# Kernel optimization log

Hardware: AMD Instinct MI355X
Metric: run time of the kernel (lower is better)

The kernel has to match this reference:

```python
import jax, jax.numpy as jnp
import numpy as np
from math import sqrt

MASK_SCALE = 128  # band half-width; entries with |i-j| < MASK_SCALE are masked to -inf

B, L, H, E = 4, 2048, 8, 64
D = 64


def setup_inputs() -> dict:
    key = jax.random.key(0)
    kq, kk, kv = jax.random.split(key, 3)
    queries = jax.random.normal(kq, (B, L, H, E), dtype=jnp.float32)
    keys = jax.random.normal(kk, (B, L, H, E), dtype=jnp.float32)
    values = jax.random.normal(kv, (B, L, H, D), dtype=jnp.float32)
    attn_mask = jnp.zeros((B, 1, L, L), dtype=bool)  # unused (mask_flag=False)
    return {"queries": queries, "keys": keys, "values": values, "attn_mask": attn_mask}


def reference(queries, keys, values, attn_mask):
    b, l, h, e = queries.shape
    scale = 1.0 / sqrt(e)
    # [B,H,L,S] dense scores
    scores = jnp.einsum('blhe,bshe->bhls', queries, keys)
    # create_diag_symmetric_mask(L, MASK_SCALE): 1 iff |i-j| < MASK_SCALE
    idx = jnp.arange(l)
    band = jnp.abs(idx[:, None] - idx[None, :]) < MASK_SCALE  # [L,L]
    # module masks the band to -inf (attends outside the band)
    scores = jnp.where(band[None, None, :, :], -jnp.inf, scores)
    A = jax.nn.softmax(scale * scores, axis=-1)
    V = jnp.einsum('bhls,bshd->blhd', A, values)
    return V
```

## Files before the change

kernel.cpp:

```cpp
#include <hip/hip_runtime.h>
#include <hip/hip_bf16.h>

typedef __bf16 bf16_t;
typedef __bf16 bf16x8 __attribute__((ext_vector_type(8)));
typedef float f32x4 __attribute__((ext_vector_type(4)));
typedef float f32x16 __attribute__((ext_vector_type(16)));
typedef unsigned int u32;

#define MFMA16(A,B,C) __builtin_amdgcn_mfma_f32_16x16x32_bf16(A,B,C,0,0,0)
#define MFMA32(A,B,C) __builtin_amdgcn_mfma_f32_32x32x16_bf16(A,B,C,0,0,0)

constexpr int Bb = 4, Ll = 2048, Hh = 8, Ee = 64, Dd = 64;
constexpr int LDP = 72;
constexpr int MS = 128;

static __device__ __forceinline__ bf16x8 cvt8(float4 a, float4 b) {
    bf16x8 t;
    t[0] = (bf16_t)a.x; t[1] = (bf16_t)a.y; t[2] = (bf16_t)a.z; t[3] = (bf16_t)a.w;
    t[4] = (bf16_t)b.x; t[5] = (bf16_t)b.y; t[6] = (bf16_t)b.z; t[7] = (bf16_t)b.w;
    return t;
}

static __device__ __forceinline__ u32 pkbf(float lo, float hi) {
    u32 d;
    asm("v_cvt_pk_bf16_f32 %0, %1, %2" : "=v"(d) : "v"(lo), "v"(hi));
    return d;
}

static __device__ __forceinline__ float fexp2(float x) {
    float r;
    asm("v_exp_f32 %0, %1" : "=v"(r) : "v"(x));
    return r;
}

static __device__ __forceinline__ f32x16 zero16() {
    f32x16 z;
    #pragma unroll
    for (int r = 0; r < 16; ++r) z[r] = 0.f;
    return z;
}

__global__ __launch_bounds__(256) void prep(const float* __restrict__ K,
                                            const float* __restrict__ V,
                                            bf16_t* __restrict__ Kb,
                                            bf16_t* __restrict__ Vt) {
    __shared__ bf16_t VLp[Dd][LDP];
    if (blockIdx.x < 2048) {
        const int c = blockIdx.x * 256 + threadIdx.x;
        const int e0 = (c & 7) * 8;
        const int h  = (c >> 3) & (Hh - 1);
        const int l  = (c >> 6) & (Ll - 1);
        const int b  = c >> 17;
        const float* s = K + ((((size_t)b * Ll + l) * Hh + h) * Ee + e0);
        float4 f0 = ((const float4*)s)[0];
        float4 f1 = ((const float4*)s)[1];
        *(bf16x8*)(Kb + ((((size_t)b * Hh + h) * Ll + l) * Ee + e0)) = cvt8(f0, f1);
    } else {
        const int bb = blockIdx.x - 2048;
        const int bh = bb >> 5;
        const int t  = bb & 31;
        const int b = bh >> 3, h = bh & 7;
        {
            const int j  = threadIdx.x >> 2;
            const int d0 = (threadIdx.x & 3) * 16;
            const float* vp = V + (((size_t)(b * Ll + t * 64 + j)) * Hh + h) * Dd + d0;
            float4 x0 = ((const float4*)vp)[0], x1 = ((const float4*)vp)[1];
            float4 x2 = ((const float4*)vp)[2], x3 = ((const float4*)vp)[3];
            VLp[d0 +  0][j] = (bf16_t)x0.x; VLp[d0 +  1][j] = (bf16_t)x0.y;
            VLp[d0 +  2][j] = (bf16_t)x0.z; VLp[d0 +  3][j] = (bf16_t)x0.w;
            VLp[d0 +  4][j] = (bf16_t)x1.x; VLp[d0 +  5][j] = (bf16_t)x1.y;
            VLp[d0 +  6][j] = (bf16_t)x1.z; VLp[d0 +  7][j] = (bf16_t)x1.w;
            VLp[d0 +  8][j] = (bf16_t)x2.x; VLp[d0 +  9][j] = (bf16_t)x2.y;
            VLp[d0 + 10][j] = (bf16_t)x2.z; VLp[d0 + 11][j] = (bf16_t)x2.w;
            VLp[d0 + 12][j] = (bf16_t)x3.x; VLp[d0 + 13][j] = (bf16_t)x3.y;
            VLp[d0 + 14][j] = (bf16_t)x3.z; VLp[d0 + 15][j] = (bf16_t)x3.w;
        }
        __syncthreads();
        {
            const int d  = threadIdx.x >> 2;
            const int j0 = (threadIdx.x & 3) * 16;
            bf16x8 a0 = *(const bf16x8*)&VLp[d][j0];
            bf16x8 a1 = *(const bf16x8*)&VLp[d][j0 + 8];
            bf16_t* op = Vt + ((((size_t)bh * 32 + t) * 64 + d) * 64 + j0);
            *(bf16x8*)op = a0;
            *(bf16x8*)(op + 8) = a1;
        }
    }
}

__global__ __launch_bounds__(256, 2) void fattn5(const float* __restrict__ Q,
                                                 const bf16_t* __restrict__ Kb,
                                                 const bf16_t* __restrict__ Vt,
                                                 float* __restrict__ O) {
    __shared__ __align__(16) bf16_t KL[2 * 8192];
    __shared__ __align__(16) bf16_t VL[2 * 8192];

    const int tid = threadIdx.x;
    const int ln  = tid & 63;
    const int wv  = tid >> 6;
    const int l31 = ln & 31;
    const int lh  = ln >> 5;

    const int bid = blockIdx.x;
    const int x   = bid & 7;
    const int o   = bid >> 3;
    const int bh  = x * 4 + (o >> 4);
    const int qt  = o & 15;
    const int q0  = qt * 128;
    const int wq0 = q0 + wv * 32;
    const int qq  = wq0 + l31;
    const int b = bh >> 3, h = bh & 7;

    const bf16_t* kbase = Kb + (size_t)bh * (Ll * 64);
    const bf16_t* vbase = Vt + (size_t)bh * (Ll * 64);

    bf16x8 qreg[4];
    {
        const float SCL2 = 0.125f * 1.44269504f;
        const float* qp = Q + (((size_t)(b * Ll + qq)) * Hh + h) * Ee + lh * 8;
        #pragma unroll
        for (int ks = 0; ks < 4; ++ks) {
            float4 f0 = *(const float4*)(qp + ks * 16);
            float4 f1 = *(const float4*)(qp + ks * 16 + 4);
            f0.x *= SCL2; f0.y *= SCL2; f0.z *= SCL2; f0.w *= SCL2;
            f1.x *= SCL2; f1.y *= SCL2; f1.z *= SCL2; f1.w *= SCL2;
            qreg[ks] = cvt8(f0, f1);
        }
    }

    bf16x8 ones;
    #pragma unroll
    for (int e = 0; e < 8; ++e) ones[e] = (bf16_t)1.0f;

    f32x16 acc0 = zero16(), acc1 = zero16(), accP = zero16();

    const int koff = (tid >> 3) * 64 + (((tid & 7) ^ ((tid >> 3) & 7)) << 3);
    const int ldst = tid * 8;

    #define STAGE(nxt, kt_) do {                                                     \
        const bf16_t* _k = kbase + (size_t)(kt_) * 8192 + koff;                      \
        const bf16_t* _v = vbase + (size_t)(kt_) * 8192 + koff;                      \
        bf16_t* _lk = KL + (nxt) * 8192 + ldst;                                      \
        bf16_t* _lv = VL + (nxt) * 8192 + ldst;                                      \
        _Pragma("unroll")                                                            \
        for (int _j = 0; _j < 4; ++_j) {                                             \
            __builtin_amdgcn_global_load_lds((const void*)(_k + _j * 2048),          \
                                             (void*)(_lk + _j * 2048), 16, 0, 0);    \
            __builtin_amdgcn_global_load_lds((const void*)(_v + _j * 2048),          \
                                             (void*)(_lv + _j * 2048), 16, 0, 0);    \
        }                                                                            \
    } while (0)

    #define SGRP(dst, g) do {                                                        \
        dst = zero16();                                                              \
        const int kb_ = bo + ((g) >> 1) * 4096 + (((g) & 1) * 32 + l31) * 64;        \
        __builtin_amdgcn_s_setprio(1);                                               \
        _Pragma("unroll")                                                            \
        for (int ks = 0; ks < 4; ++ks) {                                             \
            const int cc = (((2 * ks + lh) ^ (l31 & 7)) << 3);                       \
            bf16x8 ka = *(const bf16x8*)&KL[kb_ + cc];                               \
            dst = MFMA32(ka, qreg[ks], dst);                                         \
        }                                                                            \
        __builtin_amdgcn_s_setprio(0);                                               \
    } while (0)

    #define SMPV(g, sv) do {                                                         \
        const int kk0 = k0 + (g) * 32;                                               \
        const int dw = wq0 - kk0;                                                    \
        if (dw > -159 && dw < 159) {                                                 \
            _Pragma("unroll")                                                        \
            for (int r = 0; r < 16; ++r) {                                           \
                const int k = kk0 + 4 * lh + ((r & 3) + 8 * (r >> 2));               \
                const int dlt = qq - k;                                              \
                if (dlt > -MS && dlt < MS) sv[r] = -1e30f;                           \
            }                                                                        \
        }                                                                            \
        float p[16];                                                                 \
        _Pragma("unroll")                                                            \
        for (int r = 0; r < 16; ++r) p[r] = fexp2(sv[r]);                            \
        u32 x0 = pkbf(p[0], p[1]),   x1 = pkbf(p[2], p[3]);                          \
        u32 x2 = pkbf(p[4], p[5]),   x3 = pkbf(p[6], p[7]);                          \
        u32 x4 = pkbf(p[8], p[9]),   x5 = pkbf(p[10], p[11]);                        \
        u32 x6 = pkbf(p[12], p[13]), x7 = pkbf(p[14], p[15]);                        \
        asm volatile("v_permlane32_swap_b32 %0, %1" : "+v"(x0), "+v"(x2));           \
        asm volatile("v_permlane32_swap_b32 %0, %1" : "+v"(x1), "+v"(x3));           \
        asm volatile("v_permlane32_swap_b32 %0, %1" : "+v"(x4), "+v"(x6));           \
        asm volatile("v_permlane32_swap_b32 %0, %1" : "+v"(x5), "+v"(x7));           \
        union { u32 w[4]; bf16x8 v; } u0_, u1_;                                      \
        u0_.w[0] = x0; u0_.w[1] = x1; u0_.w[2] = x2; u0_.w[3] = x3;                  \
        u1_.w[0] = x4; u1_.w[1] = x5; u1_.w[2] = x6; u1_.w[3] = x7;                  \
        bf16x8 pf0 = u0_.v, pf1 = u1_.v;                                             \
        const int vb = bo + ((g) >> 1) * 4096;                                       \
        const int cA = (((4 * ((g) & 1) + lh) ^ (l31 & 7)) << 3);                    \
        const int cB = (((4 * ((g) & 1) + 2 + lh) ^ (l31 & 7)) << 3);                \
        bf16x8 vA0 = *(const bf16x8*)&VL[vb + l31 * 64 + cA];                        \
        bf16x8 vA1 = *(const bf16x8*)&VL[vb + (32 + l31) * 64 + cA];                 \
        bf16x8 vB0 = *(const bf16x8*)&VL[vb + l31 * 64 + cB];                        \
        bf16x8 vB1 = *(const bf16x8*)&VL[vb + (32 + l31) * 64 + cB];                 \
        __builtin_amdgcn_s_setprio(1);                                               \
        acc0 = MFMA32(pf0, vA0, acc0);                                               \
        acc1 = MFMA32(pf0, vA1, acc1);                                               \
        accP = MFMA32(pf0, ones, accP);                                              \
        acc0 = MFMA32(pf1, vB0, acc0);                                               \
        acc1 = MFMA32(pf1, vB1, acc1);                                               \
        accP = MFMA32(pf1, ones, accP);                                              \
        __builtin_amdgcn_s_setprio(0);                                               \
    } while (0)

    constexpr int NT = 15;

    STAGE(0, (0 >= qt ? 1 : 0));

    for (int i = 0; i < NT; ++i) {
        const int kt_ = i + (i >= qt ? 1 : 0);
        const int k0 = kt_ * 128;

        if (i + 1 < NT) {
            STAGE((i + 1) & 1, (i + 1) + ((i + 1) >= qt ? 1 : 0));
            asm volatile("s_waitcnt vmcnt(8)" ::: "memory");
        } else {
            asm volatile("s_waitcnt vmcnt(0)" ::: "memory");
        }
        __builtin_amdgcn_s_barrier();

        const int bo = (i & 1) * 8192;

        f32x16 sA, sB;
        SGRP(sA, 0);
        SGRP(sB, 1);
        SMPV(0, sA);
        SGRP(sA, 2);
        SMPV(1, sB);
        SGRP(sB, 3);
        SMPV(2, sA);
        SMPV(3, sB);

        __builtin_amdgcn_s_barrier();
    }
    #undef STAGE
    #undef SGRP
    #undef SMPV

    #pragma unroll
    for (int r = 0; r < 16; ++r) {
        const int rr = (r & 3) + 8 * (r >> 2) + 4 * lh;
        const float ir = 1.0f / accP[r];
        float* op = O + ((size_t)(b * Ll + wq0 + rr) * Hh + h) * Dd + l31;
        op[0]  = acc0[r] * ir;
        op[32] = acc1[r] * ir;
    }
}

__global__ __launch_bounds__(256, 2) void fattn_f32(const float* __restrict__ Q,
                                                    const float* __restrict__ K,
                                                    const float* __restrict__ V,
                                                    float* __restrict__ O) {
    __shared__ __align__(16) bf16_t Klds[64][LDP];
    __shared__ __align__(16) bf16_t Vtlds[Dd][LDP];
    __shared__ __align__(16) bf16_t Plds[4][16][LDP];

    const int tid = threadIdx.x;
    const int wv  = tid >> 6;
    const int ln  = tid & 63;
    const int l15 = ln & 15;
    const int g   = ln >> 4;

    const int nqt = Ll / 64;
    const int bid = blockIdx.x;
    const int qt  = bid % nqt;
    const int bh  = bid / nqt;
    const int b   = bh >> 3;
    const int h   = bh & 7;
    const int q0  = qt * 64;

    const float SCL2 = 0.125f * 1.44269504f;

    bf16x8 qf[2];
    {
        const float* qp = Q + (((size_t)(b * Ll + q0 + wv * 16 + l15)) * Hh + h) * Ee + g * 8;
        #pragma unroll
        for (int ks = 0; ks < 2; ++ks) {
            float4 f0 = *(const float4*)(qp + 32 * ks);
            float4 f1 = *(const float4*)(qp + 32 * ks + 4);
            qf[ks] = cvt8(f0, f1);
        }
    }

    f32x4 acc[4];
    #pragma unroll
    for (int ct = 0; ct < 4; ++ct) acc[ct] = (f32x4){0.f, 0.f, 0.f, 0.f};
    float m2[4], lsum[4];
    #pragma unroll
    for (int r = 0; r < 4; ++r) { m2[r] = -1e30f; lsum[r] = 0.f; }

    for (int k0 = 0; k0 < Ll; k0 += 64) {
        const int dd = k0 - q0;
        if (dd >= -64 && dd <= 64) continue;
        const bool needmask = (dd == 128) || (dd == -128);

        __syncthreads();
        {
            const int j  = tid >> 2;
            const int c0 = (tid & 3) << 4;
            const float* kp = K + (((size_t)(b * Ll + k0 + j)) * Hh + h) * Ee + c0;
            const float* vp = V + (((size_t)(b * Ll + k0 + j)) * Hh + h) * Dd + c0;
            float4 a0 = ((const float4*)kp)[0], a1 = ((const float4*)kp)[1];
            float4 a2 = ((const float4*)kp)[2], a3 = ((const float4*)kp)[3];
            *(bf16x8*)&Klds[j][c0]     = cvt8(a0, a1);
            *(bf16x8*)&Klds[j][c0 + 8] = cvt8(a2, a3);
            float4 b0 = ((const float4*)vp)[0], b1 = ((const float4*)vp)[1];
            float4 b2 = ((const float4*)vp)[2], b3 = ((const float4*)vp)[3];
            Vtlds[c0 +  0][j] = (bf16_t)b0.x; Vtlds[c0 +  1][j] = (bf16_t)b0.y;
            Vtlds[c0 +  2][j] = (bf16_t)b0.z; Vtlds[c0 +  3][j] = (bf16_t)b0.w;
            Vtlds[c0 +  4][j] = (bf16_t)b1.x; Vtlds[c0 +  5][j] = (bf16_t)b1.y;
            Vtlds[c0 +  6][j] = (bf16_t)b1.z; Vtlds[c0 +  7][j] = (bf16_t)b1.w;
            Vtlds[c0 +  8][j] = (bf16_t)b2.x; Vtlds[c0 +  9][j] = (bf16_t)b2.y;
            Vtlds[c0 + 10][j] = (bf16_t)b2.z; Vtlds[c0 + 11][j] = (bf16_t)b2.w;
            Vtlds[c0 + 12][j] = (bf16_t)b3.x; Vtlds[c0 + 13][j] = (bf16_t)b3.y;
            Vtlds[c0 + 14][j] = (bf16_t)b3.z; Vtlds[c0 + 15][j] = (bf16_t)b3.w;
        }
        __syncthreads();

        f32x4 s[4];
        #pragma unroll
        for (int ct = 0; ct < 4; ++ct) {
            f32x4 z = (f32x4){0.f, 0.f, 0.f, 0.f};
            #pragma unroll
            for (int ks = 0; ks < 2; ++ks) {
                bf16x8 kf = *(const bf16x8*)&Klds[ct * 16 + l15][ks * 32 + g * 8];
                z = MFMA16(qf[ks], kf, z);
            }
            s[ct] = z;
        }

        float lg[4][4];
        #pragma unroll
        for (int ct = 0; ct < 4; ++ct)
            #pragma unroll
            for (int r = 0; r < 4; ++r)
                lg[ct][r] = s[ct][r] * SCL2;

        if (needmask) {
            const int irow = q0 + wv * 16 + g * 4;
            #pragma unroll
            for (int ct = 0; ct < 4; ++ct) {
                const int j = k0 + ct * 16 + l15;
                #pragma unroll
                for (int r = 0; r < 4; ++r) {
                    int diff = irow + r - j;
                    diff = diff < 0 ? -diff : diff;
                    if (diff < MS) lg[ct][r] = -1e30f;
                }
            }
        }

        #pragma unroll
        for (int r = 0; r < 4; ++r) {
            float mx = fmaxf(fmaxf(lg[0][r], lg[1][r]), fmaxf(lg[2][r], lg[3][r]));
            #pragma unroll
            for (int off = 1; off < 16; off <<= 1) mx = fmaxf(mx, __shfl_xor(mx, off));
            const float mnew = fmaxf(m2[r], mx);
            const float c = exp2f(m2[r] - mnew);
            m2[r] = mnew;
            #pragma unroll
            for (int ct = 0; ct < 4; ++ct) acc[ct][r] *= c;
            float ps = 0.f;
            #pragma unroll
            for (int ct = 0; ct < 4; ++ct) {
                float p = exp2f(lg[ct][r] - mnew);
                bf16_t pb = (bf16_t)p;
                Plds[wv][g * 4 + r][ct * 16 + l15] = pb;
                ps += (float)pb;
            }
            #pragma unroll
            for (int off = 1; off < 16; off <<= 1) ps += __shfl_xor(ps, off);
            lsum[r] = lsum[r] * c + ps;
        }

        __syncthreads();

        #pragma unroll
        for (int ks = 0; ks < 2; ++ks) {
            bf16x8 pfr = *(const bf16x8*)&Plds[wv][l15][ks * 32 + g * 8];
            #pragma unroll
            for (int ct = 0; ct < 4; ++ct) {
                bf16x8 vf = *(const bf16x8*)&Vtlds[ct * 16 + l15][ks * 32 + g * 8];
                acc[ct] = MFMA16(pfr, vf, acc[ct]);
            }
        }
    }

    #pragma unroll
    for (int r = 0; r < 4; ++r) {
        const float inv = 1.0f / lsum[r];
        const size_t row = (size_t)(b * Ll + q0 + wv * 16 + g * 4 + r);
        float* op = O + (row * Hh + h) * Dd;
        #pragma unroll
        for (int ct = 0; ct < 4; ++ct)
            op[ct * 16 + l15] = acc[ct][r] * inv;
    }
}

extern "C" void kernel_launch(void* const* d_in, const int* in_sizes, int n_in,
                              void* d_out, int out_size, void* d_ws, size_t ws_size,
                              hipStream_t stream) {
    const float* Q = (const float*)d_in[0];
    const float* K = (const float*)d_in[1];
    const float* V = (const float*)d_in[2];
    float* O = (float*)d_out;

    const size_t nelem = (size_t)Bb * Hh * Ll * Ee;
    const size_t need  = nelem * 2 * 2;

    if (ws_size >= need) {
        bf16_t* Kb = (bf16_t*)d_ws;
        bf16_t* Vt = Kb + nelem;
        prep<<<dim3(3072), dim3(256), 0, stream>>>(K, V, Kb, Vt);
        fattn5<<<dim3(512), dim3(256), 0, stream>>>(Q, Kb, Vt, O);
    } else {
        fattn_f32<<<dim3(Bb * Hh * 32), dim3(256), 0, stream>>>(Q, K, V, O);
    }
}
```

Measured before the change: 58.37 us.

## Split KV range across two blocks per query tile and merge partial results

Adds fattn6, which gives each 128-query tile two blocks, each covering half of the unmasked key tiles. It uses smaller LDS buffers so four blocks fit per CU, and computes the row sums with an MFMA against a ones vector. The softmax uses exp2 with no running max, so the two halves' numerators and denominators can simply be added. A separate merge_o kernel sums the two halves and normalizes. This raises parallelism and occupancy, at the cost of writing and re-reading large fp32 partial buffers, one extra launch, and a risk of overflow on inputs with large scores.

```diff
diff --git a/kernel.cpp b/kernel.cpp
--- a/kernel.cpp
+++ b/kernel.cpp
@@ -13,6 +13,7 @@
 constexpr int Bb = 4, Ll = 2048, Hh = 8, Ee = 64, Dd = 64;
 constexpr int LDP = 72;
 constexpr int MS = 128;
+constexpr size_t NUMH = (size_t)32 * 2048 * 64;
 
 static __device__ __forceinline__ bf16x8 cvt8(float4 a, float4 b) {
     bf16x8 t;
@@ -86,6 +87,205 @@
             *(bf16x8*)(op + 8) = a1;
         }
     }
+}
+
+__global__ __launch_bounds__(256, 4) void fattn6(const float* __restrict__ Q,
+                                                 const bf16_t* __restrict__ Kb,
+                                                 const bf16_t* __restrict__ Vt,
+                                                 float* __restrict__ num,
+                                                 float* __restrict__ ps) {
+    __shared__ __align__(16) bf16_t KL[2 * 4096];
+    __shared__ __align__(16) bf16_t VL[2 * 4096];
+
+    const int tid = threadIdx.x;
+    const int wv  = tid >> 6;
+    const int ln  = tid & 63;
+    const int l31 = ln & 31;
+    const int lh  = ln >> 5;
+
+    const int bid = blockIdx.x;
+    const int x   = bid & 7;
+    const int o   = bid >> 3;
+    const int bh  = x * 4 + (o >> 5);
+    const int rem = o & 31;
+    const int qt  = rem >> 1;
+    const int hf  = rem & 1;
+    const int q0  = qt * 128;
+    const int wq0 = q0 + wv * 32;
+    const int qq  = wq0 + l31;
+    const int b = bh >> 3, h = bh & 7;
+
+    const bf16_t* kbase = Kb + (size_t)bh * (Ll * 64);
+    const bf16_t* vbase = Vt + (size_t)bh * (Ll * 64);
+
+    bf16x8 qreg[4];
+    {
+        const float SCL2 = 0.125f * 1.44269504f;
+        const float* qp = Q + (((size_t)(b * Ll + qq)) * Hh + h) * Ee + lh * 8;
+        #pragma unroll
+        for (int ks = 0; ks < 4; ++ks) {
+            float4 f0 = *(const float4*)(qp + ks * 16);
+            float4 f1 = *(const float4*)(qp + ks * 16 + 4);
+            f0.x *= SCL2; f0.y *= SCL2; f0.z *= SCL2; f0.w *= SCL2;
+            f1.x *= SCL2; f1.y *= SCL2; f1.z *= SCL2; f1.w *= SCL2;
+            qreg[ks] = cvt8(f0, f1);
+        }
+    }
+
+    bf16x8 ones;
+    #pragma unroll
+    for (int e = 0; e < 8; ++e) ones[e] = (bf16_t)1.0f;
+
+    f32x16 acc0 = zero16(), acc1 = zero16(), accP = zero16();
+
+    const int rowoff = (ln >> 3) * 64 + (((ln & 7) ^ (ln >> 3)) * 8);
+    const int i0 = (wv & 1) * 4;
+    const bf16_t* gsb = (wv < 2) ? kbase : vbase;
+    bf16_t* lsb = (wv < 2) ? KL : VL;
+
+    const int s0t = qt * 2;
+    const int ibeg = hf * 15;
+    const int iend = ibeg + 15;
+
+    #define STAGE(nxt, kt_) do {                                                   \
+        const bf16_t* _g = gsb + (size_t)(kt_) * 4096 + i0 * 512 + rowoff;         \
+        bf16_t* _l = lsb + (nxt) * 4096 + i0 * 512;                                \
+        _Pragma("unroll")                                                          \
+        for (int _c = 0; _c < 4; ++_c)                                             \
+            __builtin_amdgcn_global_load_lds((const void*)(_g + _c * 512),         \
+                                             (void*)(_l + _c * 512), 16, 0, 0);    \
+    } while (0)
+
+    STAGE(ibeg & 1, ibeg + (ibeg >= s0t ? 2 : 0));
+
+    for (int i = ibeg; i < iend; ++i) {
+        const int kt_ = i + (i >= s0t ? 2 : 0);
+        const int k0 = kt_ * 64;
+
+        if (i + 1 < iend) {
+            STAGE((i + 1) & 1, (i + 1) + ((i + 1) >= s0t ? 2 : 0));
+            asm volatile("s_waitcnt vmcnt(4)" ::: "memory");
+        } else {
+            asm volatile("s_waitcnt vmcnt(0)" ::: "memory");
+        }
+        __builtin_amdgcn_s_barrier();
+
+        const int bo = (i & 1) * 4096;
+
+        f32x16 s0v = zero16(), s1v = zero16();
+        __builtin_amdgcn_s_setprio(1);
+        #pragma unroll
+        for (int ks = 0; ks < 4; ++ks) {
+            const int cc = (((2 * ks + lh) ^ (l31 & 7)) << 3);
+            bf16x8 ka0 = *(const bf16x8*)&KL[bo + l31 * 64 + cc];
+            bf16x8 ka1 = *(const bf16x8*)&KL[bo + (32 + l31) * 64 + cc];
+            s0v = MFMA32(ka0, qreg[ks], s0v);
+            s1v = MFMA32(ka1, qreg[ks], s1v);
+        }
+        __builtin_amdgcn_s_setprio(0);
+
+        {
+            const int d0_ = wq0 - k0;
+            if (d0_ > -159 && d0_ < 159) {
+                #pragma unroll
+                for (int r = 0; r < 16; ++r) {
+                    const int k = k0 + 4 * lh + ((r & 3) + 8 * (r >> 2));
+                    const int dlt = qq - k;
+                    if (dlt > -MS && dlt < MS) s0v[r] = -1e30f;
+                }
+            }
+            const int d1_ = wq0 - (k0 + 32);
+            if (d1_ > -159 && d1_ < 159) {
+                #pragma unroll
+                for (int r = 0; r < 16; ++r) {
+                    const int k = k0 + 32 + 4 * lh + ((r & 3) + 8 * (r >> 2));
+                    const int dlt = qq - k;
+                    if (dlt > -MS && dlt < MS) s1v[r] = -1e30f;
+                }
+            }
+        }
+
+        bf16x8 pf[4];
+        {
+            float p[16];
+            #pragma unroll
+            for (int r = 0; r < 16; ++r) p[r] = fexp2(s0v[r]);
+            u32 x0 = pkbf(p[0], p[1]),   x1 = pkbf(p[2], p[3]);
+            u32 x2 = pkbf(p[4], p[5]),   x3 = pkbf(p[6], p[7]);
+            u32 x4 = pkbf(p[8], p[9]),   x5 = pkbf(p[10], p[11]);
+            u32 x6 = pkbf(p[12], p[13]), x7 = pkbf(p[14], p[15]);
+            asm volatile("v_permlane32_swap_b32 %0, %1" : "+v"(x0), "+v"(x2));
+            asm volatile("v_permlane32_swap_b32 %0, %1" : "+v"(x1), "+v"(x3));
+            asm volatile("v_permlane32_swap_b32 %0, %1" : "+v"(x4), "+v"(x6));
+            asm volatile("v_permlane32_swap_b32 %0, %1" : "+v"(x5), "+v"(x7));
+            union { u32 w[4]; bf16x8 v; } u0, u1;
+            u0.w[0] = x0; u0.w[1] = x1; u0.w[2] = x2; u0.w[3] = x3;
+            u1.w[0] = x4; u1.w[1] = x5; u1.w[2] = x6; u1.w[3] = x7;
+            pf[0] = u0.v; pf[1] = u1.v;
+        }
+        {
+            float p[16];
+            #pragma unroll
+            for (int r = 0; r < 16; ++r) p[r] = fexp2(s1v[r]);
+            u32 x0 = pkbf(p[0], p[1]),   x1 = pkbf(p[2], p[3]);
+            u32 x2 = pkbf(p[4], p[5]),   x3 = pkbf(p[6], p[7]);
+            u32 x4 = pkbf(p[8], p[9]),   x5 = pkbf(p[10], p[11]);
+            u32 x6 = pkbf(p[12], p[13]), x7 = pkbf(p[14], p[15]);
+            asm volatile("v_permlane32_swap_b32 %0, %1" : "+v"(x0), "+v"(x2));
+            asm volatile("v_permlane32_swap_b32 %0, %1" : "+v"(x1), "+v"(x3));
+            asm volatile("v_permlane32_swap_b32 %0, %1" : "+v"(x4), "+v"(x6));
+            asm volatile("v_permlane32_swap_b32 %0, %1" : "+v"(x5), "+v"(x7));
+            union { u32 w[4]; bf16x8 v; } u0, u1;
+            u0.w[0] = x0; u0.w[1] = x1; u0.w[2] = x2; u0.w[3] = x3;
+            u1.w[0] = x4; u1.w[1] = x5; u1.w[2] = x6; u1.w[3] = x7;
+            pf[2] = u0.v; pf[3] = u1.v;
+        }
+
+        __builtin_amdgcn_s_setprio(1);
+        #pragma unroll
+        for (int ks = 0; ks < 4; ++ks) {
+            const int cc = (((2 * ks + lh) ^ (l31 & 7)) << 3);
+            bf16x8 vf0 = *(const bf16x8*)&VL[bo + l31 * 64 + cc];
+            bf16x8 vf1 = *(const bf16x8*)&VL[bo + (32 + l31) * 64 + cc];
+            acc0 = MFMA32(pf[ks], vf0, acc0);
+            acc1 = MFMA32(pf[ks], vf1, acc1);
+            accP = MFMA32(pf[ks], ones, accP);
+        }
+        __builtin_amdgcn_s_setprio(0);
+
+        __builtin_amdgcn_s_barrier();
+    }
+    #undef STAGE
+
+    float* nh = num + (size_t)hf * NUMH + ((size_t)bh * 2048 + wq0) * 64;
+    float* ph = ps + (size_t)hf * 65536 + (size_t)bh * 2048 + wq0;
+    #pragma unroll
+    for (int r = 0; r < 16; ++r) {
+        const int rr = (r & 3) + 8 * (r >> 2) + 4 * lh;
+        float* op = nh + rr * 64 + l31;
+        op[0]  = acc0[r];
+        op[32] = acc1[r];
+        if (l31 == 0) ph[rr] = accP[r];
+    }
+}
+
+__global__ __launch_bounds__(256) void merge_o(const float* __restrict__ num,
+                                               const float* __restrict__ ps,
+                                               float* __restrict__ O) {
+    const int idx = blockIdx.x * 256 + threadIdx.x;
+    const int row = idx >> 4;
+    const int d4  = (idx & 15) << 2;
+    const float4 n0 = *(const float4*)(num + (size_t)row * 64 + d4);
+    const float4 n1 = *(const float4*)(num + NUMH + (size_t)row * 64 + d4);
+    const float inv = 1.0f / (ps[row] + ps[row + 65536]);
+    const int bh = row >> 11, l = row & 2047;
+    const int b = bh >> 3, h = bh & 7;
+    float4 o;
+    o.x = (n0.x + n1.x) * inv;
+    o.y = (n0.y + n1.y) * inv;
+    o.z = (n0.z + n1.z) * inv;
+    o.w = (n0.w + n1.w) * inv;
+    *(float4*)(O + (((size_t)(b * 2048 + l) * 8 + h) * 64 + d4)) = o;
 }
 
 __global__ __launch_bounds__(256, 2) void fattn5(const float* __restrict__ Q,
@@ -410,9 +610,18 @@
     float* O = (float*)d_out;
 
     const size_t nelem = (size_t)Bb * Hh * Ll * Ee;
-    const size_t need  = nelem * 2 * 2;
-
-    if (ws_size >= need) {
+    const size_t need1 = nelem * 2 * 2;
+    const size_t need2 = need1 + 2 * NUMH * 4 + 2 * 65536 * 4;
+
+    if (ws_size >= need2) {
+        bf16_t* Kb = (bf16_t*)d_ws;
+        bf16_t* Vt = Kb + nelem;
+        float*  num = (float*)(Vt + nelem);
+        float*  ps  = num + 2 * NUMH;
+        prep<<<dim3(3072), dim3(256), 0, stream>>>(K, V, Kb, Vt);
+        fattn6<<<dim3(1024), dim3(256), 0, stream>>>(Q, Kb, Vt, num, ps);
+        merge_o<<<dim3(4096), dim3(256), 0, stream>>>(num, ps, O);
+    } else if (ws_size >= need1) {
         bf16_t* Kb = (bf16_t*)d_ws;
         bf16_t* Vt = Kb + nelem;
         prep<<<dim3(3072), dim3(256), 0, stream>>>(K, V, Kb, Vt);
```

Measured after the change: 66.82 us. 14.5% more time.

## Replace LDS-staged K/V tiles with direct per-wave register loads and VALU row sums

Applied to the files above, without the earlier changes.

The attention kernel no longer stages K and V through double-buffered shared memory with block barriers. Each wave now loads its own 64-key K and V fragments straight from global memory into registers, ping-ponging two K register sets so the next tile's loads overlap current compute. The softmax row sum is accumulated with VALU adds plus a cross-half shuffle instead of an extra MFMA against a ones vector. This removes LDS traffic and barriers, but each of the four waves now fetches the same K/V data separately and register pressure rises, which may hurt occupancy.

```diff
diff --git a/kernel.cpp b/kernel.cpp
--- a/kernel.cpp
+++ b/kernel.cpp
@@ -88,16 +88,13 @@
     }
 }
 
-__global__ __launch_bounds__(256, 2) void fattn5(const float* __restrict__ Q,
+__global__ __launch_bounds__(256, 2) void fattn9(const float* __restrict__ Q,
                                                  const bf16_t* __restrict__ Kb,
                                                  const bf16_t* __restrict__ Vt,
                                                  float* __restrict__ O) {
-    __shared__ __align__(16) bf16_t KL[2 * 8192];
-    __shared__ __align__(16) bf16_t VL[2 * 8192];
-
     const int tid = threadIdx.x;
+    const int wv  = tid >> 6;
     const int ln  = tid & 63;
-    const int wv  = tid >> 6;
     const int l31 = ln & 31;
     const int lh  = ln >> 5;
 
@@ -113,6 +110,7 @@
 
     const bf16_t* kbase = Kb + (size_t)bh * (Ll * 64);
     const bf16_t* vbase = Vt + (size_t)bh * (Ll * 64);
+    const int loff = l31 * 64 + lh * 8;
 
     bf16x8 qreg[4];
     {
@@ -128,123 +126,134 @@
         }
     }
 
-    bf16x8 ones;
-    #pragma unroll
-    for (int e = 0; e < 8; ++e) ones[e] = (bf16_t)1.0f;
-
-    f32x16 acc0 = zero16(), acc1 = zero16(), accP = zero16();
-
-    const int koff = (tid >> 3) * 64 + (((tid & 7) ^ ((tid >> 3) & 7)) << 3);
-    const int ldst = tid * 8;
-
-    #define STAGE(nxt, kt_) do {                                                     \
-        const bf16_t* _k = kbase + (size_t)(kt_) * 8192 + koff;                      \
-        const bf16_t* _v = vbase + (size_t)(kt_) * 8192 + koff;                      \
-        bf16_t* _lk = KL + (nxt) * 8192 + ldst;                                      \
-        bf16_t* _lv = VL + (nxt) * 8192 + ldst;                                      \
-        _Pragma("unroll")                                                            \
-        for (int _j = 0; _j < 4; ++_j) {                                             \
-            __builtin_amdgcn_global_load_lds((const void*)(_k + _j * 2048),          \
-                                             (void*)(_lk + _j * 2048), 16, 0, 0);    \
-            __builtin_amdgcn_global_load_lds((const void*)(_v + _j * 2048),          \
-                                             (void*)(_lv + _j * 2048), 16, 0, 0);    \
-        }                                                                            \
+    f32x16 acc0 = zero16(), acc1 = zero16();
+    float psum = 0.f;
+
+    const int s0t = qt * 2;
+    #define TILEOF(i) ((i) + ((i) >= s0t ? 2 : 0))
+
+    bf16x8 kA[8], kB[8], vf[8];
+
+    #define LOADSET(dst, base, kt_) do {                                          \
+        const bf16_t* _p = (base) + (size_t)(kt_) * 4096 + loff;                  \
+        _Pragma("unroll")                                                         \
+        for (int _su = 0; _su < 2; ++_su)                                         \
+            _Pragma("unroll")                                                     \
+            for (int _ks = 0; _ks < 4; ++_ks)                                     \
+                dst[_su * 4 + _ks] =                                              \
+                    *(const bf16x8*)(_p + _su * 2048 + _ks * 16);                 \
     } while (0)
 
-    #define SGRP(dst, g) do {                                                        \
-        dst = zero16();                                                              \
-        const int kb_ = bo + ((g) >> 1) * 4096 + (((g) & 1) * 32 + l31) * 64;        \
-        __builtin_amdgcn_s_setprio(1);                                               \
-        _Pragma("unroll")                                                            \
-        for (int ks = 0; ks < 4; ++ks) {                                             \
-            const int cc = (((2 * ks + lh) ^ (l31 & 7)) << 3);                       \
-            bf16x8 ka = *(const bf16x8*)&KL[kb_ + cc];                               \
-            dst = MFMA32(ka, qreg[ks], dst);                                         \
-        }                                                                            \
-        __builtin_amdgcn_s_setprio(0);                                               \
+    #define TILE(kset, k0_) do {                                                  \
+        f32x16 s0v = zero16(), s1v = zero16();                                    \
+        __builtin_amdgcn_s_setprio(1);                                            \
+        _Pragma("unroll")                                                         \
+        for (int ks = 0; ks < 4; ++ks) {                                          \
+            s0v = MFMA32(kset[ks],     qreg[ks], s0v);                            \
+            s1v = MFMA32(kset[4 + ks], qreg[ks], s1v);                            \
+        }                                                                         \
+        __builtin_amdgcn_s_setprio(0);                                            \
+        {                                                                         \
+            const int d0_ = wq0 - (k0_);                                          \
+            if (d0_ > -159 && d0_ < 159) {                                        \
+                _Pragma("unroll")                                                 \
+                for (int r = 0; r < 16; ++r) {                                    \
+                    const int k = (k0_) + 4 * lh + ((r & 3) + 8 * (r >> 2));      \
+                    const int dlt = qq - k;                                       \
+                    if (dlt > -MS && dlt < MS) s0v[r] = -1e30f;                   \
+                }                                                                 \
+            }                                                                     \
+            const int d1_ = wq0 - ((k0_) + 32);                                   \
+            if (d1_ > -159 && d1_ < 159) {                                        \
+                _Pragma("unroll")                                                 \
+                for (int r = 0; r < 16; ++r) {                                    \
+                    const int k = (k0_) + 32 + 4 * lh + ((r & 3) + 8 * (r >> 2)); \
+                    const int dlt = qq - k;                                       \
+                    if (dlt > -MS && dlt < MS) s1v[r] = -1e30f;                   \
+                }                                                                 \
+            }                                                                     \
+        }                                                                         \
+        bf16x8 pf[4];                                                             \
+        {                                                                         \
+            float p[16];                                                          \
+            _Pragma("unroll")                                                     \
+            for (int r = 0; r < 16; ++r) p[r] = fexp2(s0v[r]);                    \
+            psum += ((p[0] + p[1]) + (p[2] + p[3])) +                             \
+                    ((p[4] + p[5]) + (p[6] + p[7])) +                             \
+                    (((p[8] + p[9]) + (p[10] + p[11])) +                          \
+                     ((p[12] + p[13]) + (p[14] + p[15])));                        \
+            u32 x0 = pkbf(p[0], p[1]),   x1 = pkbf(p[2], p[3]);                   \
+            u32 x2 = pkbf(p[4], p[5]),   x3 = pkbf(p[6], p[7]);                   \
+            u32 x4 = pkbf(p[8], p[9]),   x5 = pkbf(p[10], p[11]);                 \
+            u32 x6 = pkbf(p[12], p[13]), x7 = pkbf(p[14], p[15]);                 \
+            asm volatile("v_permlane32_swap_b32 %0, %1" : "+v"(x0), "+v"(x2));    \
+            asm volatile("v_permlane32_swap_b32 %0, %1" : "+v"(x1), "+v"(x3));    \
+            asm volatile("v_permlane32_swap_b32 %0, %1" : "+v"(x4), "+v"(x6));    \
+            asm volatile("v_permlane32_swap_b32 %0, %1" : "+v"(x5), "+v"(x7));    \
+            union { u32 w[4]; bf16x8 v; } u0, u1;                                 \
+            u0.w[0] = x0; u0.w[1] = x1; u0.w[2] = x2; u0.w[3] = x3;               \
+            u1.w[0] = x4; u1.w[1] = x5; u1.w[2] = x6; u1.w[3] = x7;               \
+            pf[0] = u0.v; pf[1] = u1.v;                                           \
+        }                                                                         \
+        {                                                                         \
+            float p[16];                                                          \
+            _Pragma("unroll")                                                     \
+            for (int r = 0; r < 16; ++r) p[r] = fexp2(s1v[r]);                    \
+            psum += ((p[0] + p[1]) + (p[2] + p[3])) +                             \
+                    ((p[4] + p[5]) + (p[6] + p[7])) +                             \
+                    (((p[8] + p[9]) + (p[10] + p[11])) +                          \
+                     ((p[12] + p[13]) + (p[14] + p[15])));                        \
+            u32 x0 = pkbf(p[0], p[1]),   x1 = pkbf(p[2], p[3]);                   \
+            u32 x2 = pkbf(p[4], p[5]),   x3 = pkbf(p[6], p[7]);                   \
+            u32 x4 = pkbf(p[8], p[9]),   x5 = pkbf(p[10], p[11]);                 \
+            u32 x6 = pkbf(p[12], p[13]), x7 = pkbf(p[14], p[15]);                 \
+            asm volatile("v_permlane32_swap_b32 %0, %1" : "+v"(x0), "+v"(x2));    \
+            asm volatile("v_permlane32_swap_b32 %0, %1" : "+v"(x1), "+v"(x3));    \
+            asm volatile("v_permlane32_swap_b32 %0, %1" : "+v"(x4), "+v"(x6));    \
+            asm volatile("v_permlane32_swap_b32 %0, %1" : "+v"(x5), "+v"(x7));    \
+            union { u32 w[4]; bf16x8 v; } u0, u1;                                 \
+            u0.w[0] = x0; u0.w[1] = x1; u0.w[2] = x2; u0.w[3] = x3;               \
+            u1.w[0] = x4; u1.w[1] = x5; u1.w[2] = x6; u1.w[3] = x7;               \
+            pf[2] = u0.v; pf[3] = u1.v;                                           \
+        }                                                                         \
+        __builtin_amdgcn_s_setprio(1);                                            \
+        _Pragma("unroll")                                                         \
+        for (int ks = 0; ks < 4; ++ks) {                                          \
+            acc0 = MFMA32(pf[ks], vf[ks],     acc0);                              \
+            acc1 = MFMA32(pf[ks], vf[4 + ks], acc1);                              \
+        }                                                                         \
+        __builtin_amdgcn_s_setprio(0);                                            \
     } while (0)
 
-    #define SMPV(g, sv) do {                                                         \
-        const int kk0 = k0 + (g) * 32;                                               \
-        const int dw = wq0 - kk0;                                                    \
-        if (dw > -159 && dw < 159) {                                                 \
-            _Pragma("unroll")                                                        \
-            for (int r = 0; r < 16; ++r) {                                           \
-                const int k = kk0 + 4 * lh + ((r & 3) + 8 * (r >> 2));               \
-                const int dlt = qq - k;                                              \
-                if (dlt > -MS && dlt < MS) sv[r] = -1e30f;                           \
-            }                                                                        \
-        }                                                                            \
-        float p[16];                                                                 \
-        _Pragma("unroll")                                                            \
-        for (int r = 0; r < 16; ++r) p[r] = fexp2(sv[r]);                            \
-        u32 x0 = pkbf(p[0], p[1]),   x1 = pkbf(p[2], p[3]);                          \
-        u32 x2 = pkbf(p[4], p[5]),   x3 = pkbf(p[6], p[7]);                          \
-        u32 x4 = pkbf(p[8], p[9]),   x5 = pkbf(p[10], p[11]);                        \
-        u32 x6 = pkbf(p[12], p[13]), x7 = pkbf(p[14], p[15]);                        \
-        asm volatile("v_permlane32_swap_b32 %0, %1" : "+v"(x0), "+v"(x2));           \
-        asm volatile("v_permlane32_swap_b32 %0, %1" : "+v"(x1), "+v"(x3));           \
-        asm volatile("v_permlane32_swap_b32 %0, %1" : "+v"(x4), "+v"(x6));           \
-        asm volatile("v_permlane32_swap_b32 %0, %1" : "+v"(x5), "+v"(x7));           \
-        union { u32 w[4]; bf16x8 v; } u0_, u1_;                                      \
-        u0_.w[0] = x0; u0_.w[1] = x1; u0_.w[2] = x2; u0_.w[3] = x3;                  \
-        u1_.w[0] = x4; u1_.w[1] = x5; u1_.w[2] = x6; u1_.w[3] = x7;                  \
-        bf16x8 pf0 = u0_.v, pf1 = u1_.v;                                             \
-        const int vb = bo + ((g) >> 1) * 4096;                                       \
-        const int cA = (((4 * ((g) & 1) + lh) ^ (l31 & 7)) << 3);                    \
-        const int cB = (((4 * ((g) & 1) + 2 + lh) ^ (l31 & 7)) << 3);                \
-        bf16x8 vA0 = *(const bf16x8*)&VL[vb + l31 * 64 + cA];                        \
-        bf16x8 vA1 = *(const bf16x8*)&VL[vb + (32 + l31) * 64 + cA];                 \
-        bf16x8 vB0 = *(const bf16x8*)&VL[vb + l31 * 64 + cB];                        \
-        bf16x8 vB1 = *(const bf16x8*)&VL[vb + (32 + l31) * 64 + cB];                 \
-        __builtin_amdgcn_s_setprio(1);                                               \
-        acc0 = MFMA32(pf0, vA0, acc0);                                               \
-        acc1 = MFMA32(pf0, vA1, acc1);                                               \
-        accP = MFMA32(pf0, ones, accP);                                              \
-        acc0 = MFMA32(pf1, vB0, acc0);                                               \
-        acc1 = MFMA32(pf1, vB1, acc1);                                               \
-        accP = MFMA32(pf1, ones, accP);                                              \
-        __builtin_amdgcn_s_setprio(0);                                               \
-    } while (0)
-
-    constexpr int NT = 15;
-
-    STAGE(0, (0 >= qt ? 1 : 0));
-
-    for (int i = 0; i < NT; ++i) {
-        const int kt_ = i + (i >= qt ? 1 : 0);
-        const int k0 = kt_ * 128;
-
-        if (i + 1 < NT) {
-            STAGE((i + 1) & 1, (i + 1) + ((i + 1) >= qt ? 1 : 0));
-            asm volatile("s_waitcnt vmcnt(8)" ::: "memory");
-        } else {
-            asm volatile("s_waitcnt vmcnt(0)" ::: "memory");
-        }
-        __builtin_amdgcn_s_barrier();
-
-        const int bo = (i & 1) * 8192;
-
-        f32x16 sA, sB;
-        SGRP(sA, 0);
-        SGRP(sB, 1);
-        SMPV(0, sA);
-        SGRP(sA, 2);
-        SMPV(1, sB);
-        SGRP(sB, 3);
-        SMPV(2, sA);
-        SMPV(3, sB);
-
-        __builtin_amdgcn_s_barrier();
-    }
-    #undef STAGE
-    #undef SGRP
-    #undef SMPV
-
+    LOADSET(kA, kbase, TILEOF(0));
+
+    #pragma unroll 1
+    for (int ii = 0; ii < 30; ii += 2) {
+        {
+            const int kt_ = TILEOF(ii);
+            const int k0 = kt_ * 64;
+            LOADSET(vf, vbase, kt_);
+            if (ii + 1 < 30) LOADSET(kB, kbase, TILEOF(ii + 1));
+            TILE(kA, k0);
+        }
+        {
+            const int kt_ = TILEOF(ii + 1);
+            const int k0 = kt_ * 64;
+            LOADSET(vf, vbase, kt_);
+            if (ii + 2 < 30) LOADSET(kA, kbase, TILEOF(ii + 2));
+            TILE(kB, k0);
+        }
+    }
+    #undef TILE
+    #undef LOADSET
+    #undef TILEOF
+
+    psum += __shfl_xor(psum, 32);
+    const float inv = 1.0f / psum;
     #pragma unroll
     for (int r = 0; r < 16; ++r) {
         const int rr = (r & 3) + 8 * (r >> 2) + 4 * lh;
-        const float ir = 1.0f / accP[r];
+        const float ir = __shfl(inv, rr);
         float* op = O + ((size_t)(b * Ll + wq0 + rr) * Hh + h) * Dd + l31;
         op[0]  = acc0[r] * ir;
         op[32] = acc1[r] * ir;
@@ -384,8 +393,8 @@
             bf16x8 pfr = *(const bf16x8*)&Plds[wv][l15][ks * 32 + g * 8];
             #pragma unroll
             for (int ct = 0; ct < 4; ++ct) {
-                bf16x8 vf = *(const bf16x8*)&Vtlds[ct * 16 + l15][ks * 32 + g * 8];
-                acc[ct] = MFMA16(pfr, vf, acc[ct]);
+                bf16x8 vfl = *(const bf16x8*)&Vtlds[ct * 16 + l15][ks * 32 + g * 8];
+                acc[ct] = MFMA16(pfr, vfl, acc[ct]);
             }
         }
     }
@@ -416,7 +425,7 @@
         bf16_t* Kb = (bf16_t*)d_ws;
         bf16_t* Vt = Kb + nelem;
         prep<<<dim3(3072), dim3(256), 0, stream>>>(K, V, Kb, Vt);
-        fattn5<<<dim3(512), dim3(256), 0, stream>>>(Q, Kb, Vt, O);
+        fattn9<<<dim3(512), dim3(256), 0, stream>>>(Q, Kb, Vt, O);
     } else {
         fattn_f32<<<dim3(Bb * Hh * 32), dim3(256), 0, stream>>>(Q, K, V, O);
     }
```

Result: slower. 125.8 us (+115.6%).
